# Kernel optimization log

Hardware: AMD Instinct MI355X
Metric: run time of the kernel (lower is better)

Reference implementation:

```python
import jax, jax.numpy as jnp
import numpy as np

B, T, C, H = 4, 2048, 1024, 16
D = C // H  # head_dim = 64

def setup_inputs() -> dict:
    key = jax.random.key(0)
    k1, k2, k3 = jax.random.split(key, 3)
    x = jax.random.normal(k1, (B, T, C), dtype=jnp.float32)
    W_attn = jax.random.normal(k2, (C, 3 * C), dtype=jnp.float32) * (C ** -0.5)
    b_attn = jnp.zeros((3 * C,), dtype=jnp.float32)
    W_proj = jax.random.normal(k3, (C, C), dtype=jnp.float32) * (C ** -0.5)
    b_proj = jnp.zeros((C,), dtype=jnp.float32)
    return {"x": x, "W_attn": W_attn, "b_attn": b_attn, "W_proj": W_proj, "b_proj": b_proj}

def reference(x, W_attn, b_attn, W_proj, b_proj):
    Bc, Tc, Cc = x.shape
    qkv = x @ W_attn + b_attn                       # [B,T,3C]
    q, k, v = jnp.split(qkv, 3, axis=-1)
    q = q.reshape(Bc, Tc, H, D).transpose(0, 2, 1, 3)  # [B,H,T,D]
    k = k.reshape(Bc, Tc, H, D).transpose(0, 2, 1, 3)
    v = v.reshape(Bc, Tc, H, D).transpose(0, 2, 1, 3)
    scores = jnp.einsum('bhqd,bhkd->bhqk', q, k) / jnp.sqrt(jnp.float32(D))
    causal = jnp.tril(jnp.ones((Tc, Tc), dtype=bool))
    scores = jnp.where(causal[None, None, :, :], scores, jnp.float32(-jnp.inf))
    wei = jax.nn.softmax(scores, axis=-1)           # dropout=0 -> identity
    out = jnp.einsum('bhqk,bhkd->bhqd', wei, v)     # [B,H,T,D]
    out = out.transpose(0, 2, 1, 3).reshape(Bc, Tc, Cc)
    return out @ W_proj + b_proj
```

## Files before the change

### kernel.cpp

```cpp
#include <hip/hip_runtime.h>
#include <cstdint>
#include <cstddef>

#define Bsz   4
#define Tsz   2048
#define Csz   1024
#define Hn    16
#define Dh    64
#define Mrows 8192
#define KD    1024

#define NEG_BIG (-1.0e30f)
#define SCL2  0.18033688011112042f

typedef unsigned short u16;
typedef __bf16  bf16x8 __attribute__((ext_vector_type(8)));
typedef __bf16  bf16x2 __attribute__((ext_vector_type(2)));
typedef float   f32x4  __attribute__((ext_vector_type(4)));
typedef unsigned int u32x4 __attribute__((ext_vector_type(4)));

#define BARRIER() do { asm volatile("" ::: "memory");                          \
                       __builtin_amdgcn_s_barrier();                           \
                       asm volatile("" ::: "memory"); } while (0)

template<int N> __device__ __forceinline__ void vmwait() {
  if constexpr (N >= 8)      asm volatile("s_waitcnt vmcnt(8)"  ::: "memory");
  else if constexpr (N == 4) asm volatile("s_waitcnt vmcnt(4)"  ::: "memory");
  else                       asm volatile("s_waitcnt vmcnt(0)"  ::: "memory");
}

__device__ __forceinline__ u16 f2bf(float f) {
  union { float f; unsigned int i; } v; v.f = f;
  unsigned int u = v.i;
  return (u16)((u + 0x7fffu + ((u >> 16) & 1u)) >> 16);
}
__device__ __forceinline__ unsigned int pack2bf(float a, float b) {
#if __has_builtin(__builtin_amdgcn_cvt_pk_bf16_f32)
  union { bf16x2 h; unsigned int u; } cv;
  cv.h = __builtin_amdgcn_cvt_pk_bf16_f32(a, b);
  return cv.u;
#else
  return (unsigned int)f2bf(a) | ((unsigned int)f2bf(b) << 16);
#endif
}
__device__ __forceinline__ unsigned int pack2bf_trunc(float lo, float hi) {
  return __builtin_amdgcn_perm(__builtin_bit_cast(unsigned int, hi),
                               __builtin_bit_cast(unsigned int, lo),
                               0x07060302u);
}
__device__ __forceinline__ float fast_exp2(float x) {
#if __has_builtin(__builtin_amdgcn_exp2f)
  return __builtin_amdgcn_exp2f(x);
#else
  return exp2f(x);
#endif
}

#define CVT_BLKS  (Mrows * Csz / 4 / 256)
#define TRA_BLKS  (48 * 16)
#define TRP_BLKS  (16 * 16)

__global__ __launch_bounds__(256)
void prep(const float* __restrict__ x, u16* __restrict__ xbf,
          const float* __restrict__ Wa, u16* __restrict__ WTa,
          const float* __restrict__ Wp, u16* __restrict__ WTp) {
  __shared__ u16 tile[64][65];
  int bid = blockIdx.x;
  const int tid = threadIdx.x;
  if (bid < CVT_BLKS) {
    const int i = bid * 256 + tid;
    const float4 v = ((const float4*)x)[i];
    uint2 o;
    o.x = pack2bf(v.x, v.y);
    o.y = pack2bf(v.z, v.w);
    ((uint2*)xbf)[i] = o;
    return;
  }
  bid -= CVT_BLKS;
  const float* in; u16* out; int cols, bx, by;
  if (bid < TRA_BLKS) {
    in = Wa; out = WTa; cols = 3 * Csz; bx = bid % 48; by = bid / 48;
  } else {
    bid -= TRA_BLKS;
    in = Wp; out = WTp; cols = Csz; bx = bid & 15; by = bid >> 4;
  }
  const int tc = bx * 64, tr = by * 64;
  const int xx = tid & 63, y0 = tid >> 6;
#pragma unroll
  for (int yy = 0; yy < 64; yy += 4) {
    int r = yy + y0;
    tile[r][xx] = f2bf(in[(size_t)(tr + r) * cols + tc + xx]);
  }
  __syncthreads();
#pragma unroll
  for (int yy = 0; yy < 64; yy += 4) {
    int r = yy + y0;
    out[(size_t)(tc + r) * Csz + tr + xx] = tile[xx][r];
  }
}

template<int MODE>
__global__ __launch_bounds__(256, 3)
void gemm_bt(const u16* __restrict__ A, const u16* __restrict__ BT,
             const float* __restrict__ bias, u16* __restrict__ o0,
             u16* __restrict__ o1, u16* __restrict__ o2,
             float* __restrict__ fout, int N) {
  __shared__ u16 lsA[3][128 * 32];
  __shared__ u16 lsB[3][128 * 32];
  const int tid  = threadIdx.x;
  const int lane = tid & 63;
  const int wid  = tid >> 6;
  const int wm   = wid & 1, wn = wid >> 1;
  const int quad = lane >> 4, l15 = lane & 15;
  const int rswz = (l15 >> 1) & 3;

  int bx, by;
  {
    const int nwg  = gridDim.x * gridDim.y;
    const int orig = (int)blockIdx.y * gridDim.x + (int)blockIdx.x;
    const int cpx  = nwg >> 3;
    const int swz  = (orig & 7) * cpx + (orig >> 3);
    bx = swz % gridDim.x; by = swz / gridDim.x;
  }
  const int m0 = by * 128, n0 = bx * 128;

  f32x4 acc[4][4];
#pragma unroll
  for (int i = 0; i < 4; ++i)
#pragma unroll
    for (int j = 0; j < 4; ++j) acc[i][j] = (f32x4){0.f, 0.f, 0.f, 0.f};

  const int srow   = lane >> 2;
  const int schunk = (lane & 3) ^ ((lane >> 3) & 3);
  const u16* gA = A  + (size_t)(m0 + wid * 32 + srow) * KD + schunk * 8;
  const u16* gB = BT + (size_t)(n0 + wid * 32 + srow) * KD + schunk * 8;

  auto gstage = [&](int t, int bb) {
#if __has_builtin(__builtin_amdgcn_global_load_lds)
#pragma unroll
    for (int i = 0; i < 2; ++i)
      __builtin_amdgcn_global_load_lds(
          (const __attribute__((address_space(1))) void*)(gA + (size_t)i * 16 * KD + t * 32),
          (__attribute__((address_space(3))) void*)(&lsA[bb][(wid * 32 + i * 16) * 32]),
          16, 0, 0);
#pragma unroll
    for (int i = 0; i < 2; ++i)
      __builtin_amdgcn_global_load_lds(
          (const __attribute__((address_space(1))) void*)(gB + (size_t)i * 16 * KD + t * 32),
          (__attribute__((address_space(3))) void*)(&lsB[bb][(wid * 32 + i * 16) * 32]),
          16, 0, 0);
#else
#pragma unroll
    for (int cc = 0; cc < 2; ++cc) {
      const int c = tid + cc * 256;
      const int rr = c >> 2, off = c & 3;
      const int dc = (off ^ ((rr >> 1) & 3)) << 3;
      *(uint4*)&lsA[bb][rr * 32 + dc] =
          *(const uint4*)&A[(size_t)(m0 + rr) * KD + t * 32 + off * 8];
    }
#pragma unroll
    for (int cc = 0; cc < 2; ++cc) {
      const int c = tid + cc * 256;
      const int rr = c >> 2, off = c & 3;
      const int dc = (off ^ ((rr >> 1) & 3)) << 3;
      *(uint4*)&lsB[bb][rr * 32 + dc] =
          *(const uint4*)&BT[(size_t)(n0 + rr) * KD + t * 32 + off * 8];
    }
#endif
  };

#define READ_B(n_) (*(const bf16x8*)                                           \
    &lsB[cur][(wn * 64 + (n_) * 16 + l15) * 32 + ((quad ^ rswz) << 3)])
#define READ_A(m_) (*(const bf16x8*)                                           \
    &lsA[cur][(wm * 64 + (m_) * 16 + l15) * 32 + ((quad ^ rswz) << 3)])
#define MFMA_ROW(m_, src)                                                      \
  __builtin_amdgcn_s_setprio(1);                                               \
  _Pragma("unroll")                                                            \
  for (int n = 0; n < 4; ++n)                                                  \
    acc[m_][n] = __builtin_amdgcn_mfma_f32_16x16x32_bf16(                      \
        src, bfv[n], acc[m_][n], 0, 0, 0);                                     \
  __builtin_amdgcn_s_setprio(0);

  gstage(0, 0); gstage(1, 1);
  const int KT = KD / 32;
  int cur = 0;
  for (int t = 0; t < KT; ++t) {
    if (t < KT - 1) vmwait<4>();
    else            vmwait<0>();
    BARRIER();

    if (t + 2 < KT) {
      int nb2 = cur + 2; if (nb2 >= 3) nb2 -= 3;
      gstage(t + 2, nb2);
    }

    bf16x8 bfv[4];
#pragma unroll
    for (int n = 0; n < 4; ++n) bfv[n] = READ_B(n);
    bf16x8 afA = READ_A(0);
    bf16x8 afB = READ_A(1);
    MFMA_ROW(0, afA);
    afA = READ_A(2);
    MFMA_ROW(1, afB);
    afB = READ_A(3);
    MFMA_ROW(2, afA);
    MFMA_ROW(3, afB);

    cur = (cur == 2) ? 0 : cur + 1;
  }
#undef READ_B
#undef READ_A
#undef MFMA_ROW

#pragma unroll
  for (int i = 0; i < 4; ++i) {
#pragma unroll
    for (int j = 0; j < 4; ++j) {
      const int colb = n0 + wn * 64 + j * 16 + l15;
      const float bv = bias[colb];
      float vals[4];
#pragma unroll
      for (int r = 0; r < 4; ++r) vals[r] = acc[i][j][r] + bv;
      const int row0 = m0 + wm * 64 + i * 16 + quad * 4;
      if (MODE == 0) {
        const int b = row0 >> 11, t0 = row0 & (Tsz - 1);
        const int region = colb >> 10;
        const int nc = colb & (Csz - 1);
        const int h = nc >> 6, d = nc & 63;
        if (region == 2) {
          uint2 st;
          st.x = pack2bf(vals[0], vals[1]);
          st.y = pack2bf(vals[2], vals[3]);
          *(uint2*)&o2[((size_t)((b << 4) + h) * Dh + d) * Tsz + t0] = st;
        } else {
          u16* dst = (region == 0) ? o0 : o1;
          const float qs = (region == 0) ? SCL2 : 1.0f;
#pragma unroll
          for (int r = 0; r < 4; ++r)
            dst[(size_t)(((b << 4) + h) * Tsz + t0 + r) * Dh + d] =
                f2bf(vals[r] * qs);
        }
      } else {
#pragma unroll
        for (int r = 0; r < 4; ++r)
          fout[(size_t)(row0 + r) * N + colb] = vals[r];
      }
    }
  }
}

__global__ __launch_bounds__(256)
void attn_fused(const u16* __restrict__ qb, const u16* __restrict__ kbuf,
                const u16* __restrict__ vT, u16* __restrict__ outp) {
  __shared__ u16 Kl[3][64 * 64];
  __shared__ u16 Vt[3][64 * 64];
  const int tid = threadIdx.x, lane = tid & 63, w = tid >> 6;
  const int quad = lane >> 4, l15 = lane & 15;
  const int cswz = (l15 & 7) << 3;
  const int bh = blockIdx.x;
  const int b = bh >> 4, h = bh & 15;
  const u16* Q   = qb   + (size_t)bh * Tsz * Dh;
  const u16* Kg  = kbuf + (size_t)bh * Tsz * Dh;
  const u16* VTg = vT   + (size_t)bh * Dh * Tsz;

  const int srow   = lane >> 3;
  const int schunk = ((lane & 7) ^ srow) << 3;
  const u16* gK0 = Kg  + (size_t)(w * 16 + srow) * Dh  + schunk;
  const u16* gV0 = VTg + (size_t)(w * 16 + srow) * Tsz + schunk;

#if __has_builtin(__builtin_amdgcn_global_load_lds)
#define STAGE(jj, bb) do {                                                     \
    const size_t kb_ = (size_t)(jj) * 64;                                      \
    _Pragma("unroll")                                                          \
    for (int i_ = 0; i_ < 2; ++i_) {                                           \
      __builtin_amdgcn_global_load_lds(                                        \
        (const __attribute__((address_space(1))) void*)(gK0 + (kb_ + (size_t)i_ * 8) * Dh), \
        (__attribute__((address_space(3))) void*)(&Kl[bb][(w * 16 + i_ * 8) * 64]), 16, 0, 0); \
      __builtin_amdgcn_global_load_lds(                                        \
        (const __attribute__((address_space(1))) void*)(gV0 + (size_t)(i_ * 8) * Tsz + kb_), \
        (__attribute__((address_space(3))) void*)(&Vt[bb][(w * 16 + i_ * 8) * 64]), 16, 0, 0); \
    }                                                                          \
  } while (0)
#else
#define STAGE(jj, bb) do {                                                     \
    const int kb_ = (jj) * 64;                                                 \
    _Pragma("unroll")                                                          \
    for (int cc_ = 0; cc_ < 2; ++cc_) {                                        \
      const int c_ = tid + cc_ * 256;                                          \
      const int rr_ = c_ >> 3, off_ = c_ & 7;                                  \
      const int dc_ = (off_ ^ (rr_ & 7)) << 3;                                 \
      *(uint4*)&Kl[bb][rr_ * 64 + dc_] =                                       \
          *(const uint4*)&Kg[(size_t)(kb_ + rr_) * Dh + off_ * 8];             \
      *(uint4*)&Vt[bb][rr_ * 64 + dc_] =                                       \
          *(const uint4*)&VTg[(size_t)rr_ * Tsz + kb_ + off_ * 8];             \
    }                                                                          \
  } while (0)
#endif

  for (int ph = 0; ph < 2; ++ph) {
    const int jq = ph ? (int)blockIdx.y : 31 - (int)blockIdx.y;

    const int qrow = jq * 64 + w * 16 + l15;
    const bf16x8 bq0 = *(const bf16x8*)&Q[(size_t)qrow * Dh + quad * 8];
    const bf16x8 bq1 = *(const bf16x8*)&Q[(size_t)qrow * Dh + 32 + quad * 8];

    f32x4 O[4];
#pragma unroll
    for (int nb = 0; nb < 4; ++nb) O[nb] = (f32x4){0.f, 0.f, 0.f, 0.f};
    float l_i = 0.f;

    BARRIER();
    STAGE(0, 0);
    STAGE(1, 1);

    int cur = 0;
    for (int j = 0; j <= jq; ++j) {
      if (j < jq) vmwait<4>();
      else        vmwait<0>();
      BARRIER();

      if (j + 2 <= jq) {
        int nb2 = cur + 2; if (nb2 >= 3) nb2 -= 3;
        STAGE(j + 2, nb2);
      }

      const int kb = j * 64;
      const bool diag = (j == jq);
      const int tmax = diag ? (w + 1) : 4;
      const u16* KT = Kl[cur];
      const u16* VL = Vt[cur];

      f32x4 S[4];
#pragma unroll
      for (int t = 0; t < 4; ++t) S[t] = (f32x4){0.f, 0.f, 0.f, 0.f};
      __builtin_amdgcn_s_setprio(1);
#pragma unroll
      for (int t = 0; t < 4; ++t) {
        if (t < tmax) {
          bf16x8 ak = *(const bf16x8*)&KT[(t * 16 + l15) * 64 + ((quad * 8) ^ cswz)];
          S[t] = __builtin_amdgcn_mfma_f32_16x16x32_bf16(ak, bq0, S[t], 0, 0, 0);
          ak = *(const bf16x8*)&KT[(t * 16 + l15) * 64 + ((quad * 8 + 32) ^ cswz)];
          S[t] = __builtin_amdgcn_mfma_f32_16x16x32_bf16(ak, bq1, S[t], 0, 0, 0);
        }
      }
      __builtin_amdgcn_s_setprio(0);

      float p[4][4];
      if (diag) {
#pragma unroll
        for (int t = 0; t < 4; ++t) {
          const int key0 = kb + t * 16 + quad * 4;
#pragma unroll
          for (int r = 0; r < 4; ++r) {
            const float sv =
                (t < tmax && key0 + r <= qrow) ? S[t][r] : NEG_BIG;
            p[t][r] = fast_exp2(sv);
            l_i += p[t][r];
          }
        }
      } else {
#pragma unroll
        for (int t = 0; t < 4; ++t)
#pragma unroll
          for (int r = 0; r < 4; ++r) {
            p[t][r] = fast_exp2(S[t][r]);
            l_i += p[t][r];
          }
      }

      u32x4 pu;
      pu[0] = pack2bf_trunc(p[0][0], p[0][1]);
      pu[1] = pack2bf_trunc(p[0][2], p[0][3]);
      pu[2] = pack2bf_trunc(p[1][0], p[1][1]);
      pu[3] = pack2bf_trunc(p[1][2], p[1][3]);
      bf16x8 pb = __builtin_bit_cast(bf16x8, pu);
      __builtin_amdgcn_s_setprio(1);
#pragma unroll
      for (int nb = 0; nb < 4; ++nb) {
        const uint2 a0 = *(const uint2*)&VL[(nb * 16 + l15) * 64 + ((quad * 4) ^ cswz)];
        const uint2 a1 = *(const uint2*)&VL[(nb * 16 + l15) * 64 + ((quad * 4 + 16) ^ cswz)];
        const u32x4 au = {a0.x, a0.y, a1.x, a1.y};
        O[nb] = __builtin_amdgcn_mfma_f32_16x16x32_bf16(
            __builtin_bit_cast(bf16x8, au), pb, O[nb], 0, 0, 0);
      }
      __builtin_amdgcn_s_setprio(0);
      if (tmax > 2) {
        pu[0] = pack2bf_trunc(p[2][0], p[2][1]);
        pu[1] = pack2bf_trunc(p[2][2], p[2][3]);
        pu[2] = pack2bf_trunc(p[3][0], p[3][1]);
        pu[3] = pack2bf_trunc(p[3][2], p[3][3]);
        pb = __builtin_bit_cast(bf16x8, pu);
        __builtin_amdgcn_s_setprio(1);
#pragma unroll
        for (int nb = 0; nb < 4; ++nb) {
          const uint2 a0 = *(const uint2*)&VL[(nb * 16 + l15) * 64 + ((quad * 4 + 32) ^ cswz)];
          const uint2 a1 = *(const uint2*)&VL[(nb * 16 + l15) * 64 + ((quad * 4 + 48) ^ cswz)];
          const u32x4 au = {a0.x, a0.y, a1.x, a1.y};
          O[nb] = __builtin_amdgcn_mfma_f32_16x16x32_bf16(
              __builtin_bit_cast(bf16x8, au), pb, O[nb], 0, 0, 0);
        }
        __builtin_amdgcn_s_setprio(0);
      }
      cur = (cur == 2) ? 0 : cur + 1;
    }

    float lt = l_i + __shfl_xor(l_i, 16, 64);
    lt += __shfl_xor(lt, 32, 64);
    const float inv = 1.0f / lt;
#pragma unroll
    for (int nb = 0; nb < 4; ++nb) {
      uint2 st;
      st.x = pack2bf(O[nb][0] * inv, O[nb][1] * inv);
      st.y = pack2bf(O[nb][2] * inv, O[nb][3] * inv);
      *(uint2*)&outp[(size_t)(b * Tsz + qrow) * Csz + h * Dh + nb * 16 + quad * 4] = st;
    }
  }
#undef STAGE
}

extern "C" void kernel_launch(void* const* d_in, const int* in_sizes, int n_in,
                              void* d_out, int out_size, void* d_ws, size_t ws_size,
                              hipStream_t stream) {
  const float* x      = (const float*)d_in[0];
  const float* W_attn = (const float*)d_in[1];
  const float* b_attn = (const float*)d_in[2];
  const float* W_proj = (const float*)d_in[3];
  const float* b_proj = (const float*)d_in[4];
  float* out = (float*)d_out;

  u16* ws   = (u16*)d_ws;
  u16* xbf  = ws;
  u16* qbuf = xbf  + (size_t)Mrows * Csz;
  u16* kbuf = qbuf + (size_t)Mrows * Csz;
  u16* vbuf = kbuf + (size_t)Mrows * Csz;
  u16* aout = vbuf + (size_t)Mrows * Csz;
  u16* WTa  = aout + (size_t)Mrows * Csz;
  u16* WTp  = WTa  + (size_t)Csz * 3 * Csz;

  prep<<<CVT_BLKS + TRA_BLKS + TRP_BLKS, 256, 0, stream>>>(
      x, xbf, W_attn, WTa, W_proj, WTp);
  gemm_bt<0><<<dim3(3 * Csz / 128, Mrows / 128), dim3(256), 0, stream>>>(
      xbf, WTa, b_attn, qbuf, kbuf, vbuf, nullptr, 3 * Csz);
  attn_fused<<<dim3(Bsz * Hn, Tsz / 128), 256, 0, stream>>>(
      qbuf, kbuf, vbuf, aout);
  gemm_bt<1><<<dim3(Csz / 128, Mrows / 128), dim3(256), 0, stream>>>(
      aout, WTp, b_proj, nullptr, nullptr, nullptr, out, Csz);
}
```

Before: 265.8 us.

## Process two 16-row query tiles per wave to reuse K/V tiles in attention

Each wave now handles 32 query rows (two 16-row MFMA tiles) instead of 16, so each block covers 128 query rows per phase and the grid's y dimension halves. K and V fragments loaded from LDS are shared across both query tiles, halving LDS reads and global K/V staging per query row. In exchange, register pressure roughly doubles for accumulators and scores, which may lower occupancy. There are half as many blocks (512), and causal diagonal handling becomes more branchy.

```diff
diff --git a/kernel.cpp b/kernel.cpp
--- a/kernel.cpp
+++ b/kernel.cpp
@@ -298,121 +298,189 @@
 #endif
 
   for (int ph = 0; ph < 2; ++ph) {
-    const int jq = ph ? (int)blockIdx.y : 31 - (int)blockIdx.y;
-
-    const int qrow = jq * 64 + w * 16 + l15;
-    const bf16x8 bq0 = *(const bf16x8*)&Q[(size_t)qrow * Dh + quad * 8];
-    const bf16x8 bq1 = *(const bf16x8*)&Q[(size_t)qrow * Dh + 32 + quad * 8];
-
-    f32x4 O[4];
-#pragma unroll
-    for (int nb = 0; nb < 4; ++nb) O[nb] = (f32x4){0.f, 0.f, 0.f, 0.f};
-    float l_i = 0.f;
+    const int Qi   = ph ? (int)blockIdx.y : 15 - (int)blockIdx.y;
+    const int qb0  = Qi * 128;
+    const int jmax = 2 * Qi + 1;
+    const int Q16_0 = Qi * 8 + w * 2;
+    const int qrow0 = qb0 + w * 32 + l15;
+    const int qrow1 = qrow0 + 16;
+
+    const bf16x8 bq00 = *(const bf16x8*)&Q[(size_t)qrow0 * Dh + quad * 8];
+    const bf16x8 bq01 = *(const bf16x8*)&Q[(size_t)qrow0 * Dh + 32 + quad * 8];
+    const bf16x8 bq10 = *(const bf16x8*)&Q[(size_t)qrow1 * Dh + quad * 8];
+    const bf16x8 bq11 = *(const bf16x8*)&Q[(size_t)qrow1 * Dh + 32 + quad * 8];
+
+    f32x4 O0[4], O1[4];
+#pragma unroll
+    for (int nb = 0; nb < 4; ++nb) {
+      O0[nb] = (f32x4){0.f, 0.f, 0.f, 0.f};
+      O1[nb] = (f32x4){0.f, 0.f, 0.f, 0.f};
+    }
+    float l0 = 0.f, l1 = 0.f;
 
     BARRIER();
     STAGE(0, 0);
     STAGE(1, 1);
 
     int cur = 0;
-    for (int j = 0; j <= jq; ++j) {
-      if (j < jq) vmwait<4>();
-      else        vmwait<0>();
+    for (int j = 0; j <= jmax; ++j) {
+      if (j < jmax) vmwait<4>();
+      else          vmwait<0>();
       BARRIER();
 
-      if (j + 2 <= jq) {
+      if (j + 2 <= jmax) {
         int nb2 = cur + 2; if (nb2 >= 3) nb2 -= 3;
         STAGE(j + 2, nb2);
       }
 
-      const int kb = j * 64;
-      const bool diag = (j == jq);
-      const int tmax = diag ? (w + 1) : 4;
+      const int kb   = j * 64;
+      const int rel0 = Q16_0 - 4 * j;
+      const int rel1 = rel0 + 1;
+      const int tmax0 = (rel0 >= 3) ? 4 : (rel0 + 1);
+      const int tmax1 = (rel1 >= 3) ? 4 : (rel1 + 1);
       const u16* KT = Kl[cur];
       const u16* VL = Vt[cur];
 
-      f32x4 S[4];
-#pragma unroll
-      for (int t = 0; t < 4; ++t) S[t] = (f32x4){0.f, 0.f, 0.f, 0.f};
-      __builtin_amdgcn_s_setprio(1);
-#pragma unroll
-      for (int t = 0; t < 4; ++t) {
-        if (t < tmax) {
-          bf16x8 ak = *(const bf16x8*)&KT[(t * 16 + l15) * 64 + ((quad * 8) ^ cswz)];
-          S[t] = __builtin_amdgcn_mfma_f32_16x16x32_bf16(ak, bq0, S[t], 0, 0, 0);
-          ak = *(const bf16x8*)&KT[(t * 16 + l15) * 64 + ((quad * 8 + 32) ^ cswz)];
-          S[t] = __builtin_amdgcn_mfma_f32_16x16x32_bf16(ak, bq1, S[t], 0, 0, 0);
-        }
-      }
-      __builtin_amdgcn_s_setprio(0);
-
-      float p[4][4];
-      if (diag) {
+      if (tmax1 > 0) {
+        const bool do0 = (tmax0 > 0);
+
+        f32x4 S0[4], S1[4];
 #pragma unroll
         for (int t = 0; t < 4; ++t) {
-          const int key0 = kb + t * 16 + quad * 4;
-#pragma unroll
-          for (int r = 0; r < 4; ++r) {
-            const float sv =
-                (t < tmax && key0 + r <= qrow) ? S[t][r] : NEG_BIG;
-            p[t][r] = fast_exp2(sv);
-            l_i += p[t][r];
+          S0[t] = (f32x4){0.f, 0.f, 0.f, 0.f};
+          S1[t] = (f32x4){0.f, 0.f, 0.f, 0.f};
+        }
+        __builtin_amdgcn_s_setprio(1);
+#pragma unroll
+        for (int t = 0; t < 4; ++t) {
+          if (t < tmax1) {
+            const bf16x8 ak  = *(const bf16x8*)&KT[(t * 16 + l15) * 64 + ((quad * 8) ^ cswz)];
+            const bf16x8 ak2 = *(const bf16x8*)&KT[(t * 16 + l15) * 64 + ((quad * 8 + 32) ^ cswz)];
+            if (t < tmax0) {
+              S0[t] = __builtin_amdgcn_mfma_f32_16x16x32_bf16(ak,  bq00, S0[t], 0, 0, 0);
+              S0[t] = __builtin_amdgcn_mfma_f32_16x16x32_bf16(ak2, bq01, S0[t], 0, 0, 0);
+            }
+            S1[t] = __builtin_amdgcn_mfma_f32_16x16x32_bf16(ak,  bq10, S1[t], 0, 0, 0);
+            S1[t] = __builtin_amdgcn_mfma_f32_16x16x32_bf16(ak2, bq11, S1[t], 0, 0, 0);
           }
         }
-      } else {
-#pragma unroll
-        for (int t = 0; t < 4; ++t)
-#pragma unroll
-          for (int r = 0; r < 4; ++r) {
-            p[t][r] = fast_exp2(S[t][r]);
-            l_i += p[t][r];
+        __builtin_amdgcn_s_setprio(0);
+
+        u32x4 puA1, puB1;
+        {
+          float p[4][4];
+          if (rel1 >= 4) {
+#pragma unroll
+            for (int t = 0; t < 4; ++t)
+#pragma unroll
+              for (int r = 0; r < 4; ++r) {
+                p[t][r] = fast_exp2(S1[t][r]); l1 += p[t][r];
+              }
+          } else {
+#pragma unroll
+            for (int t = 0; t < 4; ++t) {
+              const int key0 = kb + t * 16 + quad * 4;
+#pragma unroll
+              for (int r = 0; r < 4; ++r) {
+                const float sv =
+                    (t < tmax1 && key0 + r <= qrow1) ? S1[t][r] : NEG_BIG;
+                p[t][r] = fast_exp2(sv); l1 += p[t][r];
+              }
+            }
           }
-      }
-
-      u32x4 pu;
-      pu[0] = pack2bf_trunc(p[0][0], p[0][1]);
-      pu[1] = pack2bf_trunc(p[0][2], p[0][3]);
-      pu[2] = pack2bf_trunc(p[1][0], p[1][1]);
-      pu[3] = pack2bf_trunc(p[1][2], p[1][3]);
-      bf16x8 pb = __builtin_bit_cast(bf16x8, pu);
-      __builtin_amdgcn_s_setprio(1);
-#pragma unroll
-      for (int nb = 0; nb < 4; ++nb) {
-        const uint2 a0 = *(const uint2*)&VL[(nb * 16 + l15) * 64 + ((quad * 4) ^ cswz)];
-        const uint2 a1 = *(const uint2*)&VL[(nb * 16 + l15) * 64 + ((quad * 4 + 16) ^ cswz)];
-        const u32x4 au = {a0.x, a0.y, a1.x, a1.y};
-        O[nb] = __builtin_amdgcn_mfma_f32_16x16x32_bf16(
-            __builtin_bit_cast(bf16x8, au), pb, O[nb], 0, 0, 0);
-      }
-      __builtin_amdgcn_s_setprio(0);
-      if (tmax > 2) {
-        pu[0] = pack2bf_trunc(p[2][0], p[2][1]);
-        pu[1] = pack2bf_trunc(p[2][2], p[2][3]);
-        pu[2] = pack2bf_trunc(p[3][0], p[3][1]);
-        pu[3] = pack2bf_trunc(p[3][2], p[3][3]);
-        pb = __builtin_bit_cast(bf16x8, pu);
-        __builtin_amdgcn_s_setprio(1);
-#pragma unroll
-        for (int nb = 0; nb < 4; ++nb) {
-          const uint2 a0 = *(const uint2*)&VL[(nb * 16 + l15) * 64 + ((quad * 4 + 32) ^ cswz)];
-          const uint2 a1 = *(const uint2*)&VL[(nb * 16 + l15) * 64 + ((quad * 4 + 48) ^ cswz)];
-          const u32x4 au = {a0.x, a0.y, a1.x, a1.y};
-          O[nb] = __builtin_amdgcn_mfma_f32_16x16x32_bf16(
-              __builtin_bit_cast(bf16x8, au), pb, O[nb], 0, 0, 0);
-        }
-        __builtin_amdgcn_s_setprio(0);
+          puA1[0] = pack2bf_trunc(p[0][0], p[0][1]);
+          puA1[1] = pack2bf_trunc(p[0][2], p[0][3]);
+          puA1[2] = pack2bf_trunc(p[1][0], p[1][1]);
+          puA1[3] = pack2bf_trunc(p[1][2], p[1][3]);
+          puB1[0] = pack2bf_trunc(p[2][0], p[2][1]);
+          puB1[1] = pack2bf_trunc(p[2][2], p[2][3]);
+          puB1[2] = pack2bf_trunc(p[3][0], p[3][1]);
+          puB1[3] = pack2bf_trunc(p[3][2], p[3][3]);
+        }
+        u32x4 puA0 = (u32x4){0u, 0u, 0u, 0u}, puB0 = (u32x4){0u, 0u, 0u, 0u};
+        if (do0) {
+          float p[4][4];
+          if (rel0 >= 4) {
+#pragma unroll
+            for (int t = 0; t < 4; ++t)
+#pragma unroll
+              for (int r = 0; r < 4; ++r) {
+                p[t][r] = fast_exp2(S0[t][r]); l0 += p[t][r];
+              }
+          } else {
+#pragma unroll
+            for (int t = 0; t < 4; ++t) {
+              const int key0 = kb + t * 16 + quad * 4;
+#pragma unroll
+              for (int r = 0; r < 4; ++r) {
+                const float sv =
+                    (t < tmax0 && key0 + r <= qrow0) ? S0[t][r] : NEG_BIG;
+                p[t][r] = fast_exp2(sv); l0 += p[t][r];
+              }
+            }
+          }
+          puA0[0] = pack2bf_trunc(p[0][0], p[0][1]);
+          puA0[1] = pack2bf_trunc(p[0][2], p[0][3]);
+          puA0[2] = pack2bf_trunc(p[1][0], p[1][1]);
+          puA0[3] = pack2bf_trunc(p[1][2], p[1][3]);
+          puB0[0] = pack2bf_trunc(p[2][0], p[2][1]);
+          puB0[1] = pack2bf_trunc(p[2][2], p[2][3]);
+          puB0[2] = pack2bf_trunc(p[3][0], p[3][1]);
+          puB0[3] = pack2bf_trunc(p[3][2], p[3][3]);
+        }
+
+        {
+          const bf16x8 pb1 = __builtin_bit_cast(bf16x8, puA1);
+          const bf16x8 pb0 = __builtin_bit_cast(bf16x8, puA0);
+          __builtin_amdgcn_s_setprio(1);
+#pragma unroll
+          for (int nb = 0; nb < 4; ++nb) {
+            const uint2 a0 = *(const uint2*)&VL[(nb * 16 + l15) * 64 + ((quad * 4) ^ cswz)];
+            const uint2 a1 = *(const uint2*)&VL[(nb * 16 + l15) * 64 + ((quad * 4 + 16) ^ cswz)];
+            const u32x4 au = {a0.x, a0.y, a1.x, a1.y};
+            const bf16x8 av = __builtin_bit_cast(bf16x8, au);
+            O1[nb] = __builtin_amdgcn_mfma_f32_16x16x32_bf16(av, pb1, O1[nb], 0, 0, 0);
+            if (do0)
+              O0[nb] = __builtin_amdgcn_mfma_f32_16x16x32_bf16(av, pb0, O0[nb], 0, 0, 0);
+          }
+          __builtin_amdgcn_s_setprio(0);
+        }
+        if (tmax1 > 2) {
+          const bf16x8 pb1 = __builtin_bit_cast(bf16x8, puB1);
+          const bf16x8 pb0 = __builtin_bit_cast(bf16x8, puB0);
+          const bool c20 = (tmax0 > 2);
+          __builtin_amdgcn_s_setprio(1);
+#pragma unroll
+          for (int nb = 0; nb < 4; ++nb) {
+            const uint2 a0 = *(const uint2*)&VL[(nb * 16 + l15) * 64 + ((quad * 4 + 32) ^ cswz)];
+            const uint2 a1 = *(const uint2*)&VL[(nb * 16 + l15) * 64 + ((quad * 4 + 48) ^ cswz)];
+            const u32x4 au = {a0.x, a0.y, a1.x, a1.y};
+            const bf16x8 av = __builtin_bit_cast(bf16x8, au);
+            O1[nb] = __builtin_amdgcn_mfma_f32_16x16x32_bf16(av, pb1, O1[nb], 0, 0, 0);
+            if (c20)
+              O0[nb] = __builtin_amdgcn_mfma_f32_16x16x32_bf16(av, pb0, O0[nb], 0, 0, 0);
+          }
+          __builtin_amdgcn_s_setprio(0);
+        }
       }
       cur = (cur == 2) ? 0 : cur + 1;
     }
 
-    float lt = l_i + __shfl_xor(l_i, 16, 64);
-    lt += __shfl_xor(lt, 32, 64);
-    const float inv = 1.0f / lt;
+    float lt0 = l0 + __shfl_xor(l0, 16, 64);
+    lt0 += __shfl_xor(lt0, 32, 64);
+    const float inv0 = 1.0f / lt0;
+    float lt1 = l1 + __shfl_xor(l1, 16, 64);
+    lt1 += __shfl_xor(lt1, 32, 64);
+    const float inv1 = 1.0f / lt1;
 #pragma unroll
     for (int nb = 0; nb < 4; ++nb) {
       uint2 st;
-      st.x = pack2bf(O[nb][0] * inv, O[nb][1] * inv);
-      st.y = pack2bf(O[nb][2] * inv, O[nb][3] * inv);
-      *(uint2*)&outp[(size_t)(b * Tsz + qrow) * Csz + h * Dh + nb * 16 + quad * 4] = st;
+      st.x = pack2bf(O0[nb][0] * inv0, O0[nb][1] * inv0);
+      st.y = pack2bf(O0[nb][2] * inv0, O0[nb][3] * inv0);
+      *(uint2*)&outp[(size_t)(b * Tsz + qrow0) * Csz + h * Dh + nb * 16 + quad * 4] = st;
+      st.x = pack2bf(O1[nb][0] * inv1, O1[nb][1] * inv1);
+      st.y = pack2bf(O1[nb][2] * inv1, O1[nb][3] * inv1);
+      *(uint2*)&outp[(size_t)(b * Tsz + qrow1) * Csz + h * Dh + nb * 16 + quad * 4] = st;
     }
   }
 #undef STAGE
@@ -441,7 +509,7 @@
       x, xbf, W_attn, WTa, W_proj, WTp);
   gemm_bt<0><<<dim3(3 * Csz / 128, Mrows / 128), dim3(256), 0, stream>>>(
       xbf, WTa, b_attn, qbuf, kbuf, vbuf, nullptr, 3 * Csz);
-  attn_fused<<<dim3(Bsz * Hn, Tsz / 128), 256, 0, stream>>>(
+  attn_fused<<<dim3(Bsz * Hn, Tsz / 256), 256, 0, stream>>>(
       qbuf, kbuf, vbuf, aout);
   gemm_bt<1><<<dim3(Csz / 128, Mrows / 128), dim3(256), 0, stream>>>(
       aout, WTp, b_proj, nullptr, nullptr, nullptr, out, Csz);
```

New measurement: 255.3 us. -3.9%, faster.
